# Optimization experiments

Hardware: AMD Instinct MI355X
Metric: run time of the kernel (lower is better)

The kernel has to match this reference:

```python
import jax, jax.numpy as jnp
import numpy as np

B, T, E = 65536, 50, 10


def _glorot(key, shape):
    fan_in, fan_out = shape[0], shape[-1]
    limit = np.sqrt(6.0 / (fan_in + fan_out))
    return jax.random.uniform(key, shape, jnp.float32, -limit, limit)


def setup_inputs() -> dict:
    key = jax.random.key(0)
    ks = jax.random.split(key, 20)
    inp = {
        "gru_hidden_state_inputs": jax.random.normal(ks[0], (B, T, E), jnp.float32),
        "attention_s": jax.random.uniform(ks[1], (B, T, E), jnp.float32),
        # initial hidden state: GlorotUniform(shape=(1, E)) as in the TF code
        "h0": _glorot(ks[2], (1, E)),
    }
    # R_t gate (sigmoid): input_w (with bias), hidden_w (no bias), Dense_sigmoid (with bias)
    inp["Wi_r"] = _glorot(ks[3], (E, E)); inp["bi_r"] = jnp.zeros((E,), jnp.float32)
    inp["Wh_r"] = _glorot(ks[4], (E, E))
    inp["Ws_r"] = _glorot(ks[5], (E, E)); inp["bs_r"] = jnp.zeros((E,), jnp.float32)
    # Z_t gate (sigmoid)
    inp["Wi_z"] = _glorot(ks[6], (E, E)); inp["bi_z"] = jnp.zeros((E,), jnp.float32)
    inp["Wh_z"] = _glorot(ks[7], (E, E))
    inp["Ws_z"] = _glorot(ks[8], (E, E)); inp["bs_z"] = jnp.zeros((E,), jnp.float32)
    # H_t_next candidate (tanh)
    inp["Wi_h"] = _glorot(ks[9], (E, E)); inp["bi_h"] = jnp.zeros((E,), jnp.float32)
    inp["Wh_h"] = _glorot(ks[10], (E, E))
    inp["Wt_h"] = _glorot(ks[11], (E, E)); inp["bt_h"] = jnp.zeros((E,), jnp.float32)
    return inp


def reference(gru_hidden_state_inputs, attention_s, h0,
              Wi_r, bi_r, Wh_r, Ws_r, bs_r,
              Wi_z, bi_z, Wh_z, Ws_z, bs_z,
              Wi_h, bi_h, Wh_h, Wt_h, bt_h):
    b, t, e = gru_hidden_state_inputs.shape
    h = jnp.broadcast_to(h0, (b, e))  # TF broadcasts the (1,E) init against the batch
    # scan over time: xs are [T, B, E]
    xs = (jnp.swapaxes(gru_hidden_state_inputs, 0, 1),
          jnp.swapaxes(attention_s, 0, 1))

    def step(h, xa):
        x_t, a_t = xa
        # note: each gate has an EXTRA dense layer (Dense_sigmoid / Dense_tanh are Dense layers)
        r = jax.nn.sigmoid((x_t @ Wi_r + bi_r + h @ Wh_r) @ Ws_r + bs_r)
        z = jax.nn.sigmoid((x_t @ Wi_z + bi_z + h @ Wh_z) @ Ws_z + bs_z)
        hc = jnp.tanh((x_t @ Wi_h + bi_h + (h * z) @ Wh_h) @ Wt_h + bt_h)
        Ra = a_t * r
        h_next = (1.0 - Ra) * h + Ra * hc
        return h_next, None

    h_final, _ = jax.lax.scan(step, h, xs)
    return h_final
```

## Files before the change

### kernel.cpp

```cpp
#include <hip/hip_runtime.h>

#define EDIM 10
#define TDIM 50
#define BATCH 65536
#define RPB   128
#define LSTR  11

#define WTOT 640

__device__ __forceinline__ float fast_sigmoid(float x) {
    float e = __expf(-x);
    return __builtin_amdgcn_rcpf(1.0f + e);
}
__device__ __forceinline__ float fast_tanh(float x) {
    float e = __expf(2.0f * x);
    return 1.0f - 2.0f * __builtin_amdgcn_rcpf(e + 1.0f);
}

#define RL(i) __uint_as_float(__builtin_amdgcn_readlane( \
                  __float_as_uint(wreg[(i) >> 6]), (i) & 63))
#define FENCEW() asm volatile("" : "+v"(wreg[0]), "+v"(wreg[1]), "+v"(wreg[2]), \
    "+v"(wreg[3]), "+v"(wreg[4]), "+v"(wreg[5]), "+v"(wreg[6]), "+v"(wreg[7]), \
    "+v"(wreg[8]), "+v"(wreg[9]))

template<int E0>
__device__ __forceinline__ void load_a(const float* __restrict__ p, float* a) {
    if constexpr (E0 == 0) {
        float2 v0 = *(const float2*)(p + 0);
        float2 v1 = *(const float2*)(p + 2);
        a[0] = v0.x; a[1] = v0.y; a[2] = v1.x; a[3] = v1.y; a[4] = p[4];
    } else {
        a[0] = p[5];
        float2 v0 = *(const float2*)(p + 6);
        float2 v1 = *(const float2*)(p + 8);
        a[1] = v0.x; a[2] = v0.y; a[3] = v1.x; a[4] = v1.y;
    }
}

template<int E0>
__device__ __forceinline__ void augru_half(
    const float2* __restrict__ xp,
    const float*  __restrict__ ar,
    const float*  __restrict__ h0,
    float* wreg,
    float* __restrict__ hbuf, float* __restrict__ hzbuf,
    int row_l, float* __restrict__ orow)
{
    constexpr int P0 = 5 - E0;

    float h[5];
    #pragma unroll
    for (int j = 0; j < 5; j++) h[j] = h0[E0 + j];
    #pragma unroll
    for (int j = 0; j < 5; j++) hbuf[row_l * LSTR + E0 + j] = h[j];
    __syncthreads();

    float2 xc[5]; float ac[5];
    #pragma unroll
    for (int i = 0; i < 5; i++) xc[i] = xp[i];
    load_a<E0>(ar, ac);

    #pragma unroll 1
    for (int t = 0; t < TDIM; t++) {
        float hf[10];
        #pragma unroll
        for (int j = 0; j < 5; j++) {
            hf[E0 + j] = h[j];
            hf[P0 + j] = hbuf[row_l * LSTR + P0 + j];
        }

        int tn = (t < TDIM - 1) ? (t + 1) : t;
        float2 xn[5]; float an[5];
        #pragma unroll
        for (int i = 0; i < 5; i++) xn[i] = xp[tn * 5 + i];
        load_a<E0>(ar + tn * 10, an);

        float x[10];
        #pragma unroll
        for (int i = 0; i < 5; i++) { x[2 * i] = xc[i].x; x[2 * i + 1] = xc[i].y; }

        float ur[5], uz[5];
        FENCEW();
        #pragma unroll
        for (int j = 0; j < 5; j++) { ur[j] = RL(0 + E0 + j); uz[j] = RL(12 + E0 + j); }
        FENCEW();
        #pragma unroll
        for (int k = 0; k < 10; k++)
            #pragma unroll
            for (int j = 0; j < 5; j++) ur[j] = fmaf(x[k], RL(24 + k * 10 + E0 + j), ur[j]);
        FENCEW();
        #pragma unroll
        for (int k = 0; k < 10; k++)
            #pragma unroll
            for (int j = 0; j < 5; j++) uz[j] = fmaf(x[k], RL(124 + k * 10 + E0 + j), uz[j]);
        FENCEW();
        #pragma unroll
        for (int k = 0; k < 10; k++)
            #pragma unroll
            for (int j = 0; j < 5; j++) ur[j] = fmaf(hf[k], RL(224 + k * 10 + E0 + j), ur[j]);
        FENCEW();
        #pragma unroll
        for (int k = 0; k < 10; k++)
            #pragma unroll
            for (int j = 0; j < 5; j++) uz[j] = fmaf(hf[k], RL(324 + k * 10 + E0 + j), uz[j]);

        float z[5], hzo[5];
        #pragma unroll
        for (int j = 0; j < 5; j++) {
            z[j] = fast_sigmoid(uz[j]);
            hzo[j] = h[j] * z[j];
        }
        #pragma unroll
        for (int j = 0; j < 5; j++) hzbuf[row_l * LSTR + E0 + j] = hzo[j];
        __syncthreads();

        float hzf[10];
        #pragma unroll
        for (int j = 0; j < 5; j++) {
            hzf[E0 + j] = hzo[j];
            hzf[P0 + j] = hzbuf[row_l * LSTR + P0 + j];
        }

        float uh[5];
        FENCEW();
        #pragma unroll
        for (int j = 0; j < 5; j++) uh[j] = RL(424 + E0 + j);
        #pragma unroll
        for (int k = 0; k < 10; k++)
            #pragma unroll
            for (int j = 0; j < 5; j++) uh[j] = fmaf(x[k], RL(436 + k * 10 + E0 + j), uh[j]);
        FENCEW();
        #pragma unroll
        for (int k = 0; k < 10; k++)
            #pragma unroll
            for (int j = 0; j < 5; j++) uh[j] = fmaf(hzf[k], RL(536 + k * 10 + E0 + j), uh[j]);

        #pragma unroll
        for (int j = 0; j < 5; j++) {
            float r  = fast_sigmoid(ur[j]);
            float hc = fast_tanh(uh[j]);
            float Ra = ac[j] * r;
            h[j] = h[j] + Ra * (hc - h[j]);
        }

        #pragma unroll
        for (int j = 0; j < 5; j++) hbuf[row_l * LSTR + E0 + j] = h[j];
        __syncthreads();

        #pragma unroll
        for (int i = 0; i < 5; i++) xc[i] = xn[i];
        #pragma unroll
        for (int j = 0; j < 5; j++) ac[j] = an[j];
    }

    if constexpr (E0 == 0) {
        *(float2*)(orow + 0) = make_float2(h[0], h[1]);
        *(float2*)(orow + 2) = make_float2(h[2], h[3]);
        orow[4] = h[4];
    } else {
        orow[5] = h[0];
        *(float2*)(orow + 6) = make_float2(h[1], h[2]);
        *(float2*)(orow + 8) = make_float2(h[3], h[4]);
    }
}

__global__ __launch_bounds__(256, 2) void augru_main(
    const float* __restrict__ x_all, const float* __restrict__ a_all,
    const float* __restrict__ h0,
    const float* __restrict__ Wi_r, const float* __restrict__ bi_r,
    const float* __restrict__ Wh_r, const float* __restrict__ Ws_r, const float* __restrict__ bs_r,
    const float* __restrict__ Wi_z, const float* __restrict__ bi_z,
    const float* __restrict__ Wh_z, const float* __restrict__ Ws_z, const float* __restrict__ bs_z,
    const float* __restrict__ Wi_h, const float* __restrict__ bi_h,
    const float* __restrict__ Wh_h, const float* __restrict__ Wt_h, const float* __restrict__ bt_h,
    float* __restrict__ out)
{
    __shared__ __align__(16) float Wf[WTOT];
    __shared__ float hbuf[RPB * LSTR];
    __shared__ float hzbuf[RPB * LSTR];

    for (int s = threadIdx.x; s < WTOT; s += 256) {
        int g, kind, idx;
        if      (s <  12) { g = 0; kind = 0; idx = s;       }
        else if (s <  24) { g = 1; kind = 0; idx = s - 12;  }
        else if (s < 124) { g = 0; kind = 1; idx = s - 24;  }
        else if (s < 224) { g = 1; kind = 1; idx = s - 124; }
        else if (s < 324) { g = 0; kind = 2; idx = s - 224; }
        else if (s < 424) { g = 1; kind = 2; idx = s - 324; }
        else if (s < 436) { g = 2; kind = 0; idx = s - 424; }
        else if (s < 536) { g = 2; kind = 1; idx = s - 436; }
        else              { g = 2; kind = 2; idx = s - 536; }
        const float* Wi = (g == 0) ? Wi_r : (g == 1) ? Wi_z : Wi_h;
        const float* Wh = (g == 0) ? Wh_r : (g == 1) ? Wh_z : Wh_h;
        const float* Ws = (g == 0) ? Ws_r : (g == 1) ? Ws_z : Wt_h;
        const float* bi = (g == 0) ? bi_r : (g == 1) ? bi_z : bi_h;
        const float* bs = (g == 0) ? bs_r : (g == 1) ? bs_z : bt_h;
        float v = 0.0f;
        if (kind == 0) {
            if (idx < 10) {
                v = bs[idx];
                #pragma unroll
                for (int j = 0; j < 10; j++) v += bi[j] * Ws[j * 10 + idx];
            }
        } else if (idx < 100) {
            int k = idx / 10, e = idx % 10;
            const float* M = (kind == 1) ? Wi : Wh;
            #pragma unroll
            for (int j = 0; j < 10; j++) v += M[k * 10 + j] * Ws[j * 10 + e];
        }
        Wf[s] = v;
    }
    __syncthreads();

    const int lane = threadIdx.x & 63;
    float wreg[10];
    #pragma unroll
    for (int j = 0; j < 10; j++) wreg[j] = Wf[j * 64 + lane];

    const int row_l = threadIdx.x & (RPB - 1);
    const int half  = __builtin_amdgcn_readfirstlane(threadIdx.x >> 7);
    const int row   = blockIdx.x * RPB + row_l;

    const float2* xp = (const float2*)x_all + (size_t)row * (TDIM * EDIM / 2);
    const float*  ar = a_all + (size_t)row * (TDIM * EDIM);
    float* orow = out + (size_t)row * EDIM;

    if (half == 0)
        augru_half<0>(xp, ar, h0, wreg, hbuf, hzbuf, row_l, orow);
    else
        augru_half<5>(xp, ar, h0, wreg, hbuf, hzbuf, row_l, orow);
}

extern "C" void kernel_launch(void* const* d_in, const int* in_sizes, int n_in,
                              void* d_out, int out_size, void* d_ws, size_t ws_size,
                              hipStream_t stream) {
    augru_main<<<BATCH / RPB, 256, 0, stream>>>(
        (const float*)d_in[0],  (const float*)d_in[1],  (const float*)d_in[2],
        (const float*)d_in[3],  (const float*)d_in[4],  (const float*)d_in[5],
        (const float*)d_in[6],  (const float*)d_in[7],
        (const float*)d_in[8],  (const float*)d_in[9],  (const float*)d_in[10],
        (const float*)d_in[11], (const float*)d_in[12],
        (const float*)d_in[13], (const float*)d_in[14], (const float*)d_in[15],
        (const float*)d_in[16], (const float*)d_in[17],
        (float*)d_out);
}
```

Measured before the change: 397.8 us.

## Split each row's hidden state across lane halves with bpermute instead of LDS barriers

Each wavefront now handles 32 rows, and the two halves of a row's hidden state sit in lanes l and l^32. Partner values are swapped with ds_bpermute instead of LDS buffers, which removes the block-wide __syncthreads per timestep. Recurrent weights (150 floats per lane) are held in per-lane registers, while input weights are read from LDS as float4 loads instead of readlane broadcasts. The large register footprint may lower occupancy or cause spills under launch_bounds(256,2).

```diff
diff --git a/kernel.cpp b/kernel.cpp
--- a/kernel.cpp
+++ b/kernel.cpp
@@ -3,10 +3,9 @@
 #define EDIM 10
 #define TDIM 50
 #define BATCH 65536
+#define RPW   32
 #define RPB   128
-#define LSTR  11
-
-#define WTOT 640
+
 
 __device__ __forceinline__ float fast_sigmoid(float x) {
     float e = __expf(-x);
@@ -16,152 +15,8 @@
     float e = __expf(2.0f * x);
     return 1.0f - 2.0f * __builtin_amdgcn_rcpf(e + 1.0f);
 }
-
-#define RL(i) __uint_as_float(__builtin_amdgcn_readlane( \
-                  __float_as_uint(wreg[(i) >> 6]), (i) & 63))
-#define FENCEW() asm volatile("" : "+v"(wreg[0]), "+v"(wreg[1]), "+v"(wreg[2]), \
-    "+v"(wreg[3]), "+v"(wreg[4]), "+v"(wreg[5]), "+v"(wreg[6]), "+v"(wreg[7]), \
-    "+v"(wreg[8]), "+v"(wreg[9]))
-
-template<int E0>
-__device__ __forceinline__ void load_a(const float* __restrict__ p, float* a) {
-    if constexpr (E0 == 0) {
-        float2 v0 = *(const float2*)(p + 0);
-        float2 v1 = *(const float2*)(p + 2);
-        a[0] = v0.x; a[1] = v0.y; a[2] = v1.x; a[3] = v1.y; a[4] = p[4];
-    } else {
-        a[0] = p[5];
-        float2 v0 = *(const float2*)(p + 6);
-        float2 v1 = *(const float2*)(p + 8);
-        a[1] = v0.x; a[2] = v0.y; a[3] = v1.x; a[4] = v1.y;
-    }
-}
-
-template<int E0>
-__device__ __forceinline__ void augru_half(
-    const float2* __restrict__ xp,
-    const float*  __restrict__ ar,
-    const float*  __restrict__ h0,
-    float* wreg,
-    float* __restrict__ hbuf, float* __restrict__ hzbuf,
-    int row_l, float* __restrict__ orow)
-{
-    constexpr int P0 = 5 - E0;
-
-    float h[5];
-    #pragma unroll
-    for (int j = 0; j < 5; j++) h[j] = h0[E0 + j];
-    #pragma unroll
-    for (int j = 0; j < 5; j++) hbuf[row_l * LSTR + E0 + j] = h[j];
-    __syncthreads();
-
-    float2 xc[5]; float ac[5];
-    #pragma unroll
-    for (int i = 0; i < 5; i++) xc[i] = xp[i];
-    load_a<E0>(ar, ac);
-
-    #pragma unroll 1
-    for (int t = 0; t < TDIM; t++) {
-        float hf[10];
-        #pragma unroll
-        for (int j = 0; j < 5; j++) {
-            hf[E0 + j] = h[j];
-            hf[P0 + j] = hbuf[row_l * LSTR + P0 + j];
-        }
-
-        int tn = (t < TDIM - 1) ? (t + 1) : t;
-        float2 xn[5]; float an[5];
-        #pragma unroll
-        for (int i = 0; i < 5; i++) xn[i] = xp[tn * 5 + i];
-        load_a<E0>(ar + tn * 10, an);
-
-        float x[10];
-        #pragma unroll
-        for (int i = 0; i < 5; i++) { x[2 * i] = xc[i].x; x[2 * i + 1] = xc[i].y; }
-
-        float ur[5], uz[5];
-        FENCEW();
-        #pragma unroll
-        for (int j = 0; j < 5; j++) { ur[j] = RL(0 + E0 + j); uz[j] = RL(12 + E0 + j); }
-        FENCEW();
-        #pragma unroll
-        for (int k = 0; k < 10; k++)
-            #pragma unroll
-            for (int j = 0; j < 5; j++) ur[j] = fmaf(x[k], RL(24 + k * 10 + E0 + j), ur[j]);
-        FENCEW();
-        #pragma unroll
-        for (int k = 0; k < 10; k++)
-            #pragma unroll
-            for (int j = 0; j < 5; j++) uz[j] = fmaf(x[k], RL(124 + k * 10 + E0 + j), uz[j]);
-        FENCEW();
-        #pragma unroll
-        for (int k = 0; k < 10; k++)
-            #pragma unroll
-            for (int j = 0; j < 5; j++) ur[j] = fmaf(hf[k], RL(224 + k * 10 + E0 + j), ur[j]);
-        FENCEW();
-        #pragma unroll
-        for (int k = 0; k < 10; k++)
-            #pragma unroll
-            for (int j = 0; j < 5; j++) uz[j] = fmaf(hf[k], RL(324 + k * 10 + E0 + j), uz[j]);
-
-        float z[5], hzo[5];
-        #pragma unroll
-        for (int j = 0; j < 5; j++) {
-            z[j] = fast_sigmoid(uz[j]);
-            hzo[j] = h[j] * z[j];
-        }
-        #pragma unroll
-        for (int j = 0; j < 5; j++) hzbuf[row_l * LSTR + E0 + j] = hzo[j];
-        __syncthreads();
-
-        float hzf[10];
-        #pragma unroll
-        for (int j = 0; j < 5; j++) {
-            hzf[E0 + j] = hzo[j];
-            hzf[P0 + j] = hzbuf[row_l * LSTR + P0 + j];
-        }
-
-        float uh[5];
-        FENCEW();
-        #pragma unroll
-        for (int j = 0; j < 5; j++) uh[j] = RL(424 + E0 + j);
-        #pragma unroll
-        for (int k = 0; k < 10; k++)
-            #pragma unroll
-            for (int j = 0; j < 5; j++) uh[j] = fmaf(x[k], RL(436 + k * 10 + E0 + j), uh[j]);
-        FENCEW();
-        #pragma unroll
-        for (int k = 0; k < 10; k++)
-            #pragma unroll
-            for (int j = 0; j < 5; j++) uh[j] = fmaf(hzf[k], RL(536 + k * 10 + E0 + j), uh[j]);
-
-        #pragma unroll
-        for (int j = 0; j < 5; j++) {
-            float r  = fast_sigmoid(ur[j]);
-            float hc = fast_tanh(uh[j]);
-            float Ra = ac[j] * r;
-            h[j] = h[j] + Ra * (hc - h[j]);
-        }
-
-        #pragma unroll
-        for (int j = 0; j < 5; j++) hbuf[row_l * LSTR + E0 + j] = h[j];
-        __syncthreads();
-
-        #pragma unroll
-        for (int i = 0; i < 5; i++) xc[i] = xn[i];
-        #pragma unroll
-        for (int j = 0; j < 5; j++) ac[j] = an[j];
-    }
-
-    if constexpr (E0 == 0) {
-        *(float2*)(orow + 0) = make_float2(h[0], h[1]);
-        *(float2*)(orow + 2) = make_float2(h[2], h[3]);
-        orow[4] = h[4];
-    } else {
-        orow[5] = h[0];
-        *(float2*)(orow + 6) = make_float2(h[1], h[2]);
-        *(float2*)(orow + 8) = make_float2(h[3], h[4]);
-    }
+__device__ __forceinline__ float lane_xchg(int pidx, float v) {
+    return __int_as_float(__builtin_amdgcn_ds_bpermute(pidx, __float_as_int(v)));
 }
 
 __global__ __launch_bounds__(256, 2) void augru_main(
@@ -175,21 +30,15 @@
     const float* __restrict__ Wh_h, const float* __restrict__ Wt_h, const float* __restrict__ bt_h,
     float* __restrict__ out)
 {
-    __shared__ __align__(16) float Wf[WTOT];
-    __shared__ float hbuf[RPB * LSTR];
-    __shared__ float hzbuf[RPB * LSTR];
-
-    for (int s = threadIdx.x; s < WTOT; s += 256) {
-        int g, kind, idx;
-        if      (s <  12) { g = 0; kind = 0; idx = s;       }
-        else if (s <  24) { g = 1; kind = 0; idx = s - 12;  }
-        else if (s < 124) { g = 0; kind = 1; idx = s - 24;  }
-        else if (s < 224) { g = 1; kind = 1; idx = s - 124; }
-        else if (s < 324) { g = 0; kind = 2; idx = s - 224; }
-        else if (s < 424) { g = 1; kind = 2; idx = s - 324; }
-        else if (s < 436) { g = 2; kind = 0; idx = s - 424; }
-        else if (s < 536) { g = 2; kind = 1; idx = s - 436; }
-        else              { g = 2; kind = 2; idx = s - 536; }
+    __shared__ __align__(16) float WA[480];
+    __shared__ __align__(16) float WB[480];
+    __shared__ __align__(16) float WBI[48];
+
+    for (int s = threadIdx.x; s < 630; s += 256) {
+        int g, kind, k, e;
+        if (s < 30)       { kind = 0; g = s / 10;            k = 0;               e = s % 10; }
+        else if (s < 330) { kind = 1; int q = s - 30;  g = q / 100; k = (q % 100) / 10; e = q % 10; }
+        else              { kind = 2; int q = s - 330; g = q / 100; k = (q % 100) / 10; e = q % 10; }
         const float* Wi = (g == 0) ? Wi_r : (g == 1) ? Wi_z : Wi_h;
         const float* Wh = (g == 0) ? Wh_r : (g == 1) ? Wh_z : Wh_h;
         const float* Ws = (g == 0) ? Ws_r : (g == 1) ? Ws_z : Wt_h;
@@ -197,38 +46,158 @@
         const float* bs = (g == 0) ? bs_r : (g == 1) ? bs_z : bt_h;
         float v = 0.0f;
         if (kind == 0) {
-            if (idx < 10) {
-                v = bs[idx];
-                #pragma unroll
-                for (int j = 0; j < 10; j++) v += bi[j] * Ws[j * 10 + idx];
-            }
-        } else if (idx < 100) {
-            int k = idx / 10, e = idx % 10;
+            v = bs[e];
+            #pragma unroll
+            for (int j2 = 0; j2 < 10; j2++) v += bi[j2] * Ws[j2 * 10 + e];
+        } else {
             const float* M = (kind == 1) ? Wi : Wh;
             #pragma unroll
-            for (int j = 0; j < 10; j++) v += M[k * 10 + j] * Ws[j * 10 + e];
-        }
-        Wf[s] = v;
+            for (int j2 = 0; j2 < 10; j2++) v += M[k * 10 + j2] * Ws[j2 * 10 + e];
+        }
+        int hh = e / 5, j = e % 5;
+        if (kind == 0)      WBI[(g * 2 + hh) * 8 + j] = v;
+        else if (kind == 1) WA[((g * 10 + k) * 2 + hh) * 8 + j] = v;
+        else                WB[((g * 10 + k) * 2 + hh) * 8 + j] = v;
     }
     __syncthreads();
 
     const int lane = threadIdx.x & 63;
-    float wreg[10];
-    #pragma unroll
-    for (int j = 0; j < 10; j++) wreg[j] = Wf[j * 64 + lane];
-
-    const int row_l = threadIdx.x & (RPB - 1);
-    const int half  = __builtin_amdgcn_readfirstlane(threadIdx.x >> 7);
-    const int row   = blockIdx.x * RPB + row_l;
-
-    const float2* xp = (const float2*)x_all + (size_t)row * (TDIM * EDIM / 2);
-    const float*  ar = a_all + (size_t)row * (TDIM * EDIM);
-    float* orow = out + (size_t)row * EDIM;
-
-    if (half == 0)
-        augru_half<0>(xp, ar, h0, wreg, hbuf, hzbuf, row_l, orow);
-    else
-        augru_half<5>(xp, ar, h0, wreg, hbuf, hzbuf, row_l, orow);
+    const int wv   = threadIdx.x >> 6;
+    const int half = lane >> 5;
+    const int rl   = lane & 31;
+    const int row  = blockIdx.x * RPB + wv * RPW + rl;
+    const int pidx = (lane ^ 32) << 2;
+
+    float wbO[3][5][5], wbP[3][5][5];
+    #pragma unroll
+    for (int g = 0; g < 3; g++)
+        #pragma unroll
+        for (int k5 = 0; k5 < 5; k5++)
+            #pragma unroll
+            for (int j = 0; j < 5; j++) {
+                wbO[g][k5][j] = WB[((g * 10 + half * 5 + k5) * 2 + half) * 8 + j];
+                wbP[g][k5][j] = WB[((g * 10 + (1 - half) * 5 + k5) * 2 + half) * 8 + j];
+            }
+
+    const float2* xp2 = (const float2*)(x_all + (size_t)row * (TDIM * EDIM));
+    const float*  arp = a_all + (size_t)row * (TDIM * EDIM) + half * 5;
+    float* orow = out + (size_t)row * EDIM + half * 5;
+
+    float h[5], ph[5];
+    #pragma unroll
+    for (int j = 0; j < 5; j++) h[j]  = h0[half * 5 + j];
+    #pragma unroll
+    for (int j = 0; j < 5; j++) ph[j] = h0[(1 - half) * 5 + j];
+
+    float2 xc[5]; float ac[5];
+    #pragma unroll
+    for (int i = 0; i < 5; i++) xc[i] = xp2[i];
+    #pragma unroll
+    for (int j = 0; j < 5; j++) ac[j] = arp[j];
+
+    int wofs = 0;
+
+    #pragma unroll 1
+    for (int t = 0; t < TDIM; t++) {
+        asm volatile("" : "+v"(wofs));
+        const float* wa  = (const float*)WA  + half * 8 + wofs;
+        const float* wbi = (const float*)WBI + half * 8 + wofs;
+
+        int tn = (t < TDIM - 1) ? (t + 1) : t;
+        float2 xn[5]; float an[5];
+        #pragma unroll
+        for (int i = 0; i < 5; i++) xn[i] = xp2[tn * 5 + i];
+        #pragma unroll
+        for (int j = 0; j < 5; j++) an[j] = arp[tn * 10 + j];
+
+        float ur[5], uz[5];
+        {
+            float4 b4r = *(const float4*)(wbi + 0);
+            float4 b4z = *(const float4*)(wbi + 16);
+            ur[0] = b4r.x; ur[1] = b4r.y; ur[2] = b4r.z; ur[3] = b4r.w; ur[4] = wbi[4];
+            uz[0] = b4z.x; uz[1] = b4z.y; uz[2] = b4z.z; uz[3] = b4z.w; uz[4] = wbi[20];
+        }
+        #pragma unroll
+        for (int k = 0; k < 10; k++) {
+            float xk = (k & 1) ? xc[k >> 1].y : xc[k >> 1].x;
+            float4 w4 = *(const float4*)(wa + k * 16);
+            float  w1 = wa[k * 16 + 4];
+            ur[0] = fmaf(xk, w4.x, ur[0]); ur[1] = fmaf(xk, w4.y, ur[1]);
+            ur[2] = fmaf(xk, w4.z, ur[2]); ur[3] = fmaf(xk, w4.w, ur[3]);
+            ur[4] = fmaf(xk, w1,   ur[4]);
+        }
+        #pragma unroll
+        for (int k = 0; k < 10; k++) {
+            float xk = (k & 1) ? xc[k >> 1].y : xc[k >> 1].x;
+            float4 w4 = *(const float4*)(wa + 160 + k * 16);
+            float  w1 = wa[160 + k * 16 + 4];
+            uz[0] = fmaf(xk, w4.x, uz[0]); uz[1] = fmaf(xk, w4.y, uz[1]);
+            uz[2] = fmaf(xk, w4.z, uz[2]); uz[3] = fmaf(xk, w4.w, uz[3]);
+            uz[4] = fmaf(xk, w1,   uz[4]);
+        }
+        #pragma unroll
+        for (int k5 = 0; k5 < 5; k5++)
+            #pragma unroll
+            for (int j = 0; j < 5; j++) {
+                ur[j] = fmaf(h[k5], wbO[0][k5][j], ur[j]);
+                uz[j] = fmaf(h[k5], wbO[1][k5][j], uz[j]);
+            }
+        #pragma unroll
+        for (int k5 = 0; k5 < 5; k5++)
+            #pragma unroll
+            for (int j = 0; j < 5; j++) {
+                ur[j] = fmaf(ph[k5], wbP[0][k5][j], ur[j]);
+                uz[j] = fmaf(ph[k5], wbP[1][k5][j], uz[j]);
+            }
+
+        float z5[5], hzo[5], phz[5];
+        #pragma unroll
+        for (int j = 0; j < 5; j++) { z5[j] = fast_sigmoid(uz[j]); hzo[j] = h[j] * z5[j]; }
+        #pragma unroll
+        for (int j = 0; j < 5; j++) phz[j] = lane_xchg(pidx, hzo[j]);
+
+        float uh[5];
+        {
+            float4 b4h = *(const float4*)(wbi + 32);
+            uh[0] = b4h.x; uh[1] = b4h.y; uh[2] = b4h.z; uh[3] = b4h.w; uh[4] = wbi[36];
+        }
+        #pragma unroll
+        for (int k = 0; k < 10; k++) {
+            float xk = (k & 1) ? xc[k >> 1].y : xc[k >> 1].x;
+            float4 w4 = *(const float4*)(wa + 320 + k * 16);
+            float  w1 = wa[320 + k * 16 + 4];
+            uh[0] = fmaf(xk, w4.x, uh[0]); uh[1] = fmaf(xk, w4.y, uh[1]);
+            uh[2] = fmaf(xk, w4.z, uh[2]); uh[3] = fmaf(xk, w4.w, uh[3]);
+            uh[4] = fmaf(xk, w1,   uh[4]);
+        }
+        #pragma unroll
+        for (int k5 = 0; k5 < 5; k5++)
+            #pragma unroll
+            for (int j = 0; j < 5; j++) uh[j] = fmaf(hzo[k5], wbO[2][k5][j], uh[j]);
+        #pragma unroll
+        for (int k5 = 0; k5 < 5; k5++)
+            #pragma unroll
+            for (int j = 0; j < 5; j++) uh[j] = fmaf(phz[k5], wbP[2][k5][j], uh[j]);
+
+        #pragma unroll
+        for (int j = 0; j < 5; j++) {
+            float r  = fast_sigmoid(ur[j]);
+            float hc = fast_tanh(uh[j]);
+            float Ra = ac[j] * r;
+            h[j] = fmaf(Ra, hc - h[j], h[j]);
+        }
+
+        #pragma unroll
+        for (int j = 0; j < 5; j++) ph[j] = lane_xchg(pidx, h[j]);
+
+        #pragma unroll
+        for (int i = 0; i < 5; i++) xc[i] = xn[i];
+        #pragma unroll
+        for (int j = 0; j < 5; j++) ac[j] = an[j];
+    }
+
+    #pragma unroll
+    for (int j = 0; j < 5; j++) orow[j] = h[j];
 }
 
 extern "C" void kernel_launch(void* const* d_in, const int* in_sizes, int n_in,
```

New measurement: 343.0 us. -13.8%, faster.
